# Performance work log

Measured on AMD Instinct MI355X. Metric: run time of the kernel, lower is better.

## Reference

```python
import jax, jax.numpy as jnp
import numpy as np

N = 100_000      # nodes
E = 3_200_000    # edges (before self-loops)
IN_DIM = 256
H1, H2 = 64, 32
OUT_DIM = 40
NEG_SLOPE = 0.2  # PyG GATConv default


def setup_inputs() -> dict:
    key = jax.random.key(0)
    ks = jax.random.split(key, 12)
    s = 0.05
    return {
        "x": jax.random.normal(ks[0], (N, IN_DIM), jnp.float32),
        "edge_index": jax.random.randint(ks[1], (2, E), 0, N, jnp.int32),
        "W1": jax.random.normal(ks[2], (IN_DIM, H1), jnp.float32) * s,
        "att_src1": jax.random.normal(ks[3], (H1,), jnp.float32) * s,
        "att_dst1": jax.random.normal(ks[4], (H1,), jnp.float32) * s,
        "b1": jnp.zeros((H1,), jnp.float32),
        "W2": jax.random.normal(ks[5], (H1, H2), jnp.float32) * s,
        "att_src2": jax.random.normal(ks[6], (H2,), jnp.float32) * s,
        "att_dst2": jax.random.normal(ks[7], (H2,), jnp.float32) * s,
        "b2": jnp.zeros((H2,), jnp.float32),
        "fcW": jax.random.normal(ks[8], (H2, OUT_DIM), jnp.float32) * s,
        "fcb": jnp.zeros((OUT_DIM,), jnp.float32),
    }


def gat_conv(x, src, dst, W, a_src, a_dst, b):
    """Single-head PyG GATConv (concat, heads=1). src/dst already include self-loops."""
    n = x.shape[0]
    h = x @ W                                   # [N, C] projected features (lin has no bias)
    alpha_s = (h * a_src).sum(-1)               # [N]
    alpha_d = (h * a_dst).sum(-1)               # [N]
    logit = jax.nn.leaky_relu(alpha_s[src] + alpha_d[dst], NEG_SLOPE)  # [E']
    # segment softmax over edges grouped by destination node
    m = jax.ops.segment_max(logit, dst, num_segments=n)               # [N]
    e = jnp.exp(logit - m[dst])                                        # [E']
    denom = jax.ops.segment_sum(e, dst, num_segments=n)               # [N]
    alpha = e / denom[dst]                                             # [E']
    out = jax.ops.segment_sum(h[src] * alpha[:, None], dst, num_segments=n)  # [N, C]
    return out + b


def reference(x, edge_index, W1, att_src1, att_dst1, b1, W2, att_src2, att_dst2, b2, fcW, fcb):
    n = x.shape[0]
    # add_self_loops=True (PyG GATConv default)
    loop = jnp.arange(n, dtype=edge_index.dtype)
    src = jnp.concatenate([edge_index[0], loop])
    dst = jnp.concatenate([edge_index[1], loop])
    h = jax.nn.relu(gat_conv(x, src, dst, W1, att_src1, att_dst1, b1))
    emb = jax.nn.relu(gat_conv(h, src, dst, W2, att_src2, att_dst2, b2))
    logits = emb @ fcW + fcb
    return emb, logits
```

## Files before the change

### kernel.cpp

```cpp
#include <hip/hip_runtime.h>
#include <hip/hip_bf16.h>

#define NEG_SLOPE 0.2f
#define IN_DIM 256
#define C1 64
#define C2 32
#define ODIM 40
#define SCAN_CHUNK 4096
#define BSHIFT 12
#define ECHUNK 8192
#define ECH2 16384
#define CH 10

typedef unsigned short ushort16;

__device__ __forceinline__ unsigned bf16_rne(float f) {
    unsigned a = __float_as_uint(f);
    return (a + 0x7FFFu + ((a >> 16) & 1u)) >> 16;
}
__device__ __forceinline__ void bf16x2_unpack(unsigned u, float& f0, float& f1) {
    f0 = __uint_as_float(u << 16);
    f1 = __uint_as_float(u & 0xFFFF0000u);
}


__global__ void k_bhist(const int* __restrict__ dst, int E, int* __restrict__ gh,
                        int nblk, int nb) {
    __shared__ int h[32];
    int t = threadIdx.x;
    if (t < 32) h[t] = 0;
    __syncthreads();
    int base = blockIdx.x * ECHUNK;
    int end = min(base + ECHUNK, E);
    for (int i = base + t; i < end; i += 256) atomicAdd(&h[dst[i] >> BSHIFT], 1);
    __syncthreads();
    if (t < nb) gh[t * nblk + blockIdx.x] = h[t];
}

__global__ void k_bscan(int* __restrict__ gh, int L) {
    __shared__ int lds[256];
    __shared__ int carry;
    int t = threadIdx.x;
    if (t == 0) carry = 0;
    __syncthreads();
    for (int base = 0; base < L; base += 256) {
        int v = (base + t < L) ? gh[base + t] : 0;
        lds[t] = v; __syncthreads();
        for (int off = 1; off < 256; off <<= 1) {
            int u = (t >= off) ? lds[t - off] : 0;
            __syncthreads();
            lds[t] += u;
            __syncthreads();
        }
        if (base + t < L) gh[base + t] = lds[t] - v + carry;
        __syncthreads();
        if (t == 0) carry += lds[255];
        __syncthreads();
    }
}

__global__ void k_bplace(const int* __restrict__ src, const int* __restrict__ dst, int E,
                         const int* __restrict__ gh, int nblk, int nb,
                         int2* __restrict__ pairs) {
    __shared__ int cur[32];
    int t = threadIdx.x;
    if (t < nb) cur[t] = gh[t * nblk + blockIdx.x];
    __syncthreads();
    int base = blockIdx.x * ECHUNK;
    int end = min(base + ECHUNK, E);
    for (int i = base + t; i < end; i += 256) {
        int d = dst[i];
        int pos = atomicAdd(&cur[d >> BSHIFT], 1);
        pairs[pos] = make_int2(src[i], d);
    }
}

__device__ __forceinline__ void bc_map(int blk, int* b, int* c) {
    int xcd = blk & 7, k = blk >> 3;
    *b = (k & 3) * 8 + xcd;
    *c = k >> 2;
}

__global__ __launch_bounds__(512)
void k_nhist(const int2* __restrict__ pairs, const int* __restrict__ gh, int nblk,
             int nb, int E, int* __restrict__ chist) {
    __shared__ int h[4096];
    int b, c; bc_map(blockIdx.x, &b, &c);
    if (b >= nb) return;
    for (int i = threadIdx.x; i < 4096; i += 512) h[i] = 0;
    __syncthreads();
    int estart = gh[b * nblk];
    int eend = (b + 1 < nb) ? gh[(b + 1) * nblk] : E;
    int s0 = estart + c * ECH2;
    int s1 = min(s0 + ECH2, eend);
    for (int i = s0 + threadIdx.x; i < s1; i += 512)
        atomicAdd(&h[pairs[i].y & 4095], 1);
    __syncthreads();
    int* out = chist + ((size_t)b * CH + c) * 4096;
    for (int i = threadIdx.x; i < 4096; i += 512) out[i] = h[i];
}

__global__ void k_cnt(const int* __restrict__ chist, int* __restrict__ cnt, int n) {
    int i = blockIdx.x * 256 + threadIdx.x;
    if (i >= n) return;
    int b = i >> BSHIFT, j = i & 4095;
    const int* p = chist + ((size_t)b * CH) * 4096 + j;
    int s = 1;
#pragma unroll
    for (int c = 0; c < CH; c++) s += p[c * 4096];
    cnt[i] = s;
}

__global__ void k_scan1(const int* __restrict__ cnt, int n, int* __restrict__ bsums) {
    __shared__ int lds[256];
    int t = threadIdx.x;
    int base = blockIdx.x * SCAN_CHUNK + t * 16;
    int s = 0;
#pragma unroll
    for (int i = 0; i < 16; i++) { int idx = base + i; s += (idx < n) ? cnt[idx] : 0; }
    lds[t] = s; __syncthreads();
    for (int off = 128; off > 0; off >>= 1) {
        if (t < off) lds[t] += lds[t + off];
        __syncthreads();
    }
    if (t == 0) bsums[blockIdx.x] = lds[0];
}

__global__ void k_scan2(int* bsums, int nb, int* row_ptr, int n, int total) {
    __shared__ int lds[256];
    int t = threadIdx.x;
    int v = (t < nb) ? bsums[t] : 0;
    lds[t] = v; __syncthreads();
    for (int off = 1; off < 256; off <<= 1) {
        int u = (t >= off) ? lds[t - off] : 0;
        __syncthreads();
        lds[t] += u;
        __syncthreads();
    }
    if (t < nb) bsums[t] = lds[t] - v;
    if (t == 0) row_ptr[n] = total;
}

__global__ void k_scan3(const int* __restrict__ cnt, int n, const int* __restrict__ bsums,
                        int* __restrict__ row_ptr) {
    __shared__ int lds[256];
    int t = threadIdx.x;
    int base = blockIdx.x * SCAN_CHUNK + t * 16;
    int loc[16];
    int s = 0;
#pragma unroll
    for (int i = 0; i < 16; i++) {
        int idx = base + i;
        int c = (idx < n) ? cnt[idx] : 0;
        loc[i] = s; s += c;
    }
    lds[t] = s; __syncthreads();
    for (int off = 1; off < 256; off <<= 1) {
        int u = (t >= off) ? lds[t - off] : 0;
        __syncthreads();
        lds[t] += u;
        __syncthreads();
    }
    int texcl = lds[t] - s + bsums[blockIdx.x];
#pragma unroll
    for (int i = 0; i < 16; i++) {
        int idx = base + i;
        if (idx < n) row_ptr[idx] = texcl + loc[i];
    }
}

__global__ void k_selfloop(const int* __restrict__ row_ptr, int n, int* __restrict__ adj) {
    int i = blockIdx.x * 256 + threadIdx.x;
    if (i < n) adj[row_ptr[i]] = i;
}

__global__ void k_nscan(int* __restrict__ chist, const int* __restrict__ row_ptr, int n) {
    int i = blockIdx.x * 256 + threadIdx.x;
    if (i >= n) return;
    int b = i >> BSHIFT, j = i & 4095;
    int* p = chist + ((size_t)b * CH) * 4096 + j;
    int s = row_ptr[i] + 1;
#pragma unroll
    for (int c = 0; c < CH; c++) { int t = p[c * 4096]; p[c * 4096] = s; s += t; }
}

__global__ __launch_bounds__(512)
void k_place2(const int2* __restrict__ pairs, const int* __restrict__ gh, int nblk,
              int nb, int E, const int* __restrict__ chist, int* __restrict__ adj) {
    __shared__ int cur[4096];
    int b, c; bc_map(blockIdx.x, &b, &c);
    if (b >= nb) return;
    const int* cs = chist + ((size_t)b * CH + c) * 4096;
    for (int i = threadIdx.x; i < 4096; i += 512) cur[i] = cs[i];
    __syncthreads();
    int estart = gh[b * nblk];
    int eend = (b + 1 < nb) ? gh[(b + 1) * nblk] : E;
    int s0 = estart + c * ECH2;
    int s1 = min(s0 + ECH2, eend);
    for (int i = s0 + threadIdx.x; i < s1; i += 512) {
        int2 p = pairs[i];
        int pos = atomicAdd(&cur[p.y & 4095], 1);
        adj[pos] = p.x;
    }
}


__global__ __launch_bounds__(256, 4)
void k_gemm1(const float* __restrict__ x, const float* __restrict__ W1,
             const float* __restrict__ attS, const float* __restrict__ attD,
             ushort16* __restrict__ h1b, float* __restrict__ asP,
             float* __restrict__ adP, int n) {
    int t = threadIdx.x;
    int wave = t >> 6, lane = t & 63;
    int half = blockIdx.x & 1;
    int chalf = half * 32;
    int row = (blockIdx.x >> 1) * 256 + wave * 64 + lane;
    bool active = row < n;
    int rowc = active ? row : n - 1;
    const float4* xr = (const float4*)(x + (size_t)rowc * IN_DIM);

    float acc[32];
#pragma unroll
    for (int c = 0; c < 32; c++) acc[c] = 0.f;

#define FMA_K(XC, KK) { \
        const float* wk = wb + (KK) * C1; \
        _Pragma("unroll") \
        for (int c = 0; c < 32; c++) acc[c] = fmaf((XC), wk[c], acc[c]); }

    for (int k0 = 0; k0 < 16; k0++) {
        float4 xv0 = xr[k0 * 4 + 0];
        float4 xv1 = xr[k0 * 4 + 1];
        float4 xv2 = xr[k0 * 4 + 2];
        float4 xv3 = xr[k0 * 4 + 3];
        const float* wb = W1 + (size_t)(k0 * 16) * C1 + chalf;
        FMA_K(xv0.x, 0)  FMA_K(xv0.y, 1)  FMA_K(xv0.z, 2)  FMA_K(xv0.w, 3)
        FMA_K(xv1.x, 4)  FMA_K(xv1.y, 5)  FMA_K(xv1.z, 6)  FMA_K(xv1.w, 7)
        FMA_K(xv2.x, 8)  FMA_K(xv2.y, 9)  FMA_K(xv2.z, 10) FMA_K(xv2.w, 11)
        FMA_K(xv3.x, 12) FMA_K(xv3.y, 13) FMA_K(xv3.z, 14) FMA_K(xv3.w, 15)
    }
#undef FMA_K

    if (!active) return;
    float vs = 0.f, vd = 0.f;
#pragma unroll
    for (int c = 0; c < 32; c++) {
        vs = fmaf(acc[c], attS[chalf + c], vs);
        vd = fmaf(acc[c], attD[chalf + c], vd);
    }
    asP[half * n + row] = vs;
    adP[half * n + row] = vd;

    uint4* hp = (uint4*)((ushort16*)h1b + (size_t)row * C1 + chalf);
#pragma unroll
    for (int j = 0; j < 4; j++) {
        unsigned p0 = bf16_rne(acc[j*8+0]) | (bf16_rne(acc[j*8+1]) << 16);
        unsigned p1 = bf16_rne(acc[j*8+2]) | (bf16_rne(acc[j*8+3]) << 16);
        unsigned p2 = bf16_rne(acc[j*8+4]) | (bf16_rne(acc[j*8+5]) << 16);
        unsigned p3 = bf16_rne(acc[j*8+6]) | (bf16_rne(acc[j*8+7]) << 16);
        hp[j] = make_uint4(p0, p1, p2, p3);
    }
}

__global__ void k_alphaC(const float* __restrict__ asP, const float* __restrict__ adP,
                         float* __restrict__ as1, float* __restrict__ ad1, int n) {
    int i = blockIdx.x * 256 + threadIdx.x;
    if (i < n) {
        as1[i] = asP[i] + asP[n + i];
        ad1[i] = adP[i] + adP[n + i];
    }
}


__global__ __launch_bounds__(256)
void k_agg1(const ushort16* __restrict__ h1b, const float* __restrict__ as1,
            const float* __restrict__ ad1, const int* __restrict__ row_ptr,
            const int* __restrict__ adj, const float* __restrict__ b1,
            float* __restrict__ h1out, int n) {
    int wave = (blockIdx.x * 256 + threadIdx.x) >> 6;
    int lane = threadIdx.x & 63;
    if (wave >= n) return;
    int d = wave;
    int beg = row_ptr[d], end = row_ptr[d + 1];
    float adv = ad1[d];
    int g = lane >> 3, cq = lane & 7;
    float acc[8];
#pragma unroll
    for (int k = 0; k < 8; k++) acc[k] = 0.f;
    float dsum = 0.f;

#define AGG1_ROUND(E_) { \
        int se = __shfl(s, (E_)); \
        float we = __shfl(w, (E_)); \
        uint4 u = ((const uint4*)(h1b + (size_t)se * C1))[cq]; \
        float f0, f1; \
        bf16x2_unpack(u.x, f0, f1); acc[0]=fmaf(we,f0,acc[0]); acc[1]=fmaf(we,f1,acc[1]); \
        bf16x2_unpack(u.y, f0, f1); acc[2]=fmaf(we,f0,acc[2]); acc[3]=fmaf(we,f1,acc[3]); \
        bf16x2_unpack(u.z, f0, f1); acc[4]=fmaf(we,f0,acc[4]); acc[5]=fmaf(we,f1,acc[5]); \
        bf16x2_unpack(u.w, f0, f1); acc[6]=fmaf(we,f0,acc[6]); acc[7]=fmaf(we,f1,acc[7]); }

    for (int base = beg; base < end; base += 64) {
        int cnt = min(64, end - base);
        int s = d; float w = 0.f;
        if (lane < cnt) {
            s = adj[base + lane];
            float lg = as1[s] + adv;
            lg = lg > 0.f ? lg : NEG_SLOPE * lg;
            w = expf(lg);
            dsum += w;
        }
        int j = 0;
        for (; j + 32 <= cnt; j += 32) {
            AGG1_ROUND(j + g)
            AGG1_ROUND(j + 8 + g)
            AGG1_ROUND(j + 16 + g)
            AGG1_ROUND(j + 24 + g)
        }
        for (; j < cnt; j += 8) AGG1_ROUND(j + g)
    }
#undef AGG1_ROUND

#pragma unroll
    for (int off = 32; off > 0; off >>= 1) dsum += __shfl_xor(dsum, off);
#pragma unroll
    for (int off = 8; off <= 32; off <<= 1) {
#pragma unroll
        for (int k = 0; k < 8; k++) acc[k] += __shfl_xor(acc[k], off);
    }
    if (g == 0) {
        float inv = 1.f / dsum;
        float4 bv0 = ((const float4*)b1)[cq * 2];
        float4 bv1 = ((const float4*)b1)[cq * 2 + 1];
        float4 o0, o1;
        o0.x = acc[0] * inv + bv0.x; o0.x = o0.x > 0.f ? o0.x : 0.f;
        o0.y = acc[1] * inv + bv0.y; o0.y = o0.y > 0.f ? o0.y : 0.f;
        o0.z = acc[2] * inv + bv0.z; o0.z = o0.z > 0.f ? o0.z : 0.f;
        o0.w = acc[3] * inv + bv0.w; o0.w = o0.w > 0.f ? o0.w : 0.f;
        o1.x = acc[4] * inv + bv1.x; o1.x = o1.x > 0.f ? o1.x : 0.f;
        o1.y = acc[5] * inv + bv1.y; o1.y = o1.y > 0.f ? o1.y : 0.f;
        o1.z = acc[6] * inv + bv1.z; o1.z = o1.z > 0.f ? o1.z : 0.f;
        o1.w = acc[7] * inv + bv1.w; o1.w = o1.w > 0.f ? o1.w : 0.f;
        float4* op = (float4*)(h1out + (size_t)d * C1 + cq * 8);
        op[0] = o0; op[1] = o1;
    }
}


__global__ __launch_bounds__(256)
void k_gemm2(const float* __restrict__ h1out, const float* __restrict__ W2,
             const float* __restrict__ attS, const float* __restrict__ attD,
             ushort16* __restrict__ h2b, float* __restrict__ as2,
             float* __restrict__ ad2, int n) {
    __shared__ float w2t[C2 * 68];
    __shared__ float sAttS[C2], sAttD[C2];
    int t = threadIdx.x;
    for (int i = t; i < C1 * C2; i += 256) {
        int k = i >> 5, c = i & 31;
        w2t[c * 68 + k] = W2[i];
    }
    if (t < C2) { sAttS[t] = attS[t]; sAttD[t] = attD[t]; }
    __syncthreads();
    int wave = t >> 6, lane = t & 63;
    int col = lane & 31, half = lane >> 5;
    int rowbase = blockIdx.x * 32 + wave * 8;
    const float* wrow = &w2t[col * 68];
    for (int rr = 0; rr < 8; rr += 2) {
        int row = rowbase + rr + half;
        if (row >= n) return;
        float acc = 0.f;
#pragma unroll
        for (int k = 0; k < C1; k += 4) {
            float4 wv = *(const float4*)&wrow[k];
            float4 xv = *(const float4*)&h1out[(size_t)row * C1 + k];
            acc = fmaf(xv.x, wv.x, acc);
            acc = fmaf(xv.y, wv.y, acc);
            acc = fmaf(xv.z, wv.z, acc);
            acc = fmaf(xv.w, wv.w, acc);
        }
        h2b[(size_t)row * C2 + col] = (ushort16)bf16_rne(acc);
        float vs = acc * sAttS[col], vd = acc * sAttD[col];
#pragma unroll
        for (int off = 16; off > 0; off >>= 1) {
            vs += __shfl_xor(vs, off);
            vd += __shfl_xor(vd, off);
        }
        if (col == 0) { as2[row] = vs; ad2[row] = vd; }
    }
}


__global__ __launch_bounds__(256)
void k_agg2(const ushort16* __restrict__ h2b, const float* __restrict__ as2,
            const float* __restrict__ ad2, const int* __restrict__ row_ptr,
            const int* __restrict__ adj, const float* __restrict__ b2,
            float* __restrict__ emb, int n) {
    int wave = (blockIdx.x * 256 + threadIdx.x) >> 6;
    int lane = threadIdx.x & 63;
    if (wave >= n) return;
    int d = wave;
    int beg = row_ptr[d], end = row_ptr[d + 1];
    float adv = ad2[d];
    int g = lane >> 2, cq = lane & 3;
    float acc[8];
#pragma unroll
    for (int k = 0; k < 8; k++) acc[k] = 0.f;
    float dsum = 0.f;

#define AGG2_ROUND(E_) { \
        int se = __shfl(s, (E_)); \
        float we = __shfl(w, (E_)); \
        uint4 u = ((const uint4*)(h2b + (size_t)se * C2))[cq]; \
        float f0, f1; \
        bf16x2_unpack(u.x, f0, f1); acc[0]=fmaf(we,f0,acc[0]); acc[1]=fmaf(we,f1,acc[1]); \
        bf16x2_unpack(u.y, f0, f1); acc[2]=fmaf(we,f0,acc[2]); acc[3]=fmaf(we,f1,acc[3]); \
        bf16x2_unpack(u.z, f0, f1); acc[4]=fmaf(we,f0,acc[4]); acc[5]=fmaf(we,f1,acc[5]); \
        bf16x2_unpack(u.w, f0, f1); acc[6]=fmaf(we,f0,acc[6]); acc[7]=fmaf(we,f1,acc[7]); }

    for (int base = beg; base < end; base += 64) {
        int cnt = min(64, end - base);
        int s = d; float w = 0.f;
        if (lane < cnt) {
            s = adj[base + lane];
            float lg = as2[s] + adv;
            lg = lg > 0.f ? lg : NEG_SLOPE * lg;
            w = expf(lg);
            dsum += w;
        }
        int j = 0;
        for (; j + 64 <= cnt; j += 64) {
            AGG2_ROUND(j + g)
            AGG2_ROUND(j + 16 + g)
            AGG2_ROUND(j + 32 + g)
            AGG2_ROUND(j + 48 + g)
        }
        for (; j < cnt; j += 16) AGG2_ROUND(j + g)
    }
#undef AGG2_ROUND

#pragma unroll
    for (int off = 32; off > 0; off >>= 1) dsum += __shfl_xor(dsum, off);
#pragma unroll
    for (int off = 4; off <= 32; off <<= 1) {
#pragma unroll
        for (int k = 0; k < 8; k++) acc[k] += __shfl_xor(acc[k], off);
    }
    if (g == 0) {
        float inv = 1.f / dsum;
        float4 bv0 = ((const float4*)b2)[cq * 2];
        float4 bv1 = ((const float4*)b2)[cq * 2 + 1];
        float4 o0, o1;
        o0.x = acc[0] * inv + bv0.x; o0.x = o0.x > 0.f ? o0.x : 0.f;
        o0.y = acc[1] * inv + bv0.y; o0.y = o0.y > 0.f ? o0.y : 0.f;
        o0.z = acc[2] * inv + bv0.z; o0.z = o0.z > 0.f ? o0.z : 0.f;
        o0.w = acc[3] * inv + bv0.w; o0.w = o0.w > 0.f ? o0.w : 0.f;
        o1.x = acc[4] * inv + bv1.x; o1.x = o1.x > 0.f ? o1.x : 0.f;
        o1.y = acc[5] * inv + bv1.y; o1.y = o1.y > 0.f ? o1.y : 0.f;
        o1.z = acc[6] * inv + bv1.z; o1.z = o1.z > 0.f ? o1.z : 0.f;
        o1.w = acc[7] * inv + bv1.w; o1.w = o1.w > 0.f ? o1.w : 0.f;
        float4* op = (float4*)(emb + (size_t)d * C2 + cq * 8);
        op[0] = o0; op[1] = o1;
    }
}


__global__ __launch_bounds__(256)
void k_logits(const float* __restrict__ emb, const float* __restrict__ fcW,
              const float* __restrict__ fcb, float* __restrict__ out, int n) {
    __shared__ float w[C2 * ODIM];
    __shared__ float b[ODIM];
    int t = threadIdx.x;
    for (int i = t; i < C2 * ODIM; i += 256) w[i] = fcW[i];
    if (t < ODIM) b[t] = fcb[t];
    __syncthreads();
    int lane = t & 63;
    int row = blockIdx.x * 4 + (t >> 6);
    if (row >= n) return;
    float acc = (lane < ODIM) ? b[lane] : 0.f;
    const float4* er = (const float4*)&emb[(size_t)row * C2];
#pragma unroll
    for (int c4 = 0; c4 < 8; c4++) {
        float4 e = er[c4];
        int c = c4 * 4;
        if (lane < ODIM) {
            acc = fmaf(e.x, w[(c + 0) * ODIM + lane], acc);
            acc = fmaf(e.y, w[(c + 1) * ODIM + lane], acc);
            acc = fmaf(e.z, w[(c + 2) * ODIM + lane], acc);
            acc = fmaf(e.w, w[(c + 3) * ODIM + lane], acc);
        }
    }
    if (lane < ODIM) out[(size_t)row * ODIM + lane] = acc;
}


extern "C" void kernel_launch(void* const* d_in, const int* in_sizes, int n_in,
                              void* d_out, int out_size, void* d_ws, size_t ws_size,
                              hipStream_t stream) {
    const float* x    = (const float*)d_in[0];
    const int*   ei   = (const int*)d_in[1];
    const float* W1   = (const float*)d_in[2];
    const float* aS1  = (const float*)d_in[3];
    const float* aD1  = (const float*)d_in[4];
    const float* b1   = (const float*)d_in[5];
    const float* W2   = (const float*)d_in[6];
    const float* aS2  = (const float*)d_in[7];
    const float* aD2  = (const float*)d_in[8];
    const float* b2   = (const float*)d_in[9];
    const float* fcW  = (const float*)d_in[10];
    const float* fcb  = (const float*)d_in[11];

    const int N = in_sizes[0] / IN_DIM;
    const int E = in_sizes[1] / 2;
    const int* src = ei;
    const int* dst = ei + E;

    ushort16* h1b = (ushort16*)d_ws;
    float* h1out  = (float*)((char*)d_ws + (size_t)N * C1 * 2);
    float* as1    = h1out + (size_t)N * C1;
    float* ad1    = as1 + N;
    float* as2    = ad1 + N;
    float* ad2    = as2 + N;
    float* asP    = ad2 + N;
    float* adP    = asP + 2 * (size_t)N;
    int*   cnt    = (int*)(adP + 2 * (size_t)N);
    int*   row_ptr = cnt + N;
    int*   bsums   = row_ptr + (N + 1);
    int*   adj     = bsums + 256;
    int*   gh      = adj + (E + N);

    int2* pairs = (int2*)h1out;
    int*  chist = (int*)h1b;
    ushort16* h2b = (ushort16*)h1b;

    float* emb    = (float*)d_out;
    float* logits = emb + (size_t)N * C2;

    int nbN   = (N + 255) / 256;
    int nbS   = (N + SCAN_CHUNK - 1) / SCAN_CHUNK;
    int nblkE = (E + ECHUNK - 1) / ECHUNK;
    int nb    = (N + (1 << BSHIFT) - 1) >> BSHIFT;
    int nBC   = 8 * 4 * CH;

    k_bhist<<<nblkE, 256, 0, stream>>>(dst, E, gh, nblkE, nb);
    k_bscan<<<1, 256, 0, stream>>>(gh, nb * nblkE);
    k_bplace<<<nblkE, 256, 0, stream>>>(src, dst, E, gh, nblkE, nb, pairs);
    k_nhist<<<nBC, 512, 0, stream>>>(pairs, gh, nblkE, nb, E, chist);
    k_cnt<<<nbN, 256, 0, stream>>>(chist, cnt, N);
    k_scan1<<<nbS, 256, 0, stream>>>(cnt, N, bsums);
    k_scan2<<<1, 256, 0, stream>>>(bsums, nbS, row_ptr, N, E + N);
    k_scan3<<<nbS, 256, 0, stream>>>(cnt, N, bsums, row_ptr);
    k_selfloop<<<nbN, 256, 0, stream>>>(row_ptr, N, adj);
    k_nscan<<<nbN, 256, 0, stream>>>(chist, row_ptr, N);
    k_place2<<<nBC, 512, 0, stream>>>(pairs, gh, nblkE, nb, E, chist, adj);

    int nbG1 = 2 * ((N + 255) / 256);
    k_gemm1<<<nbG1, 256, 0, stream>>>(x, W1, aS1, aD1, h1b, asP, adP, N);
    k_alphaC<<<nbN, 256, 0, stream>>>(asP, adP, as1, ad1, N);
    int nbA = (N + 3) / 4;
    k_agg1<<<nbA, 256, 0, stream>>>(h1b, as1, ad1, row_ptr, adj, b1, h1out, N);
    int nbG2 = (N + 31) / 32;
    k_gemm2<<<nbG2, 256, 0, stream>>>(h1out, W2, aS2, aD2, h2b, as2, ad2, N);
    k_agg2<<<nbA, 256, 0, stream>>>(h2b, as2, ad2, row_ptr, adj, b2, emb, N);
    k_logits<<<nbA, 256, 0, stream>>>(emb, fcW, fcb, logits, N);
}
```

Before: 409.7 us.

## Stage x tiles in LDS so both column halves share one global read

```diff
diff --git a/kernel.cpp b/kernel.cpp
--- a/kernel.cpp
+++ b/kernel.cpp
@@ -210,36 +210,51 @@
              const float* __restrict__ attS, const float* __restrict__ attD,
              ushort16* __restrict__ h1b, float* __restrict__ asP,
              float* __restrict__ adP, int n) {
+    __shared__ float xs[128 * 33];
     int t = threadIdx.x;
     int wave = t >> 6, lane = t & 63;
-    int half = blockIdx.x & 1;
+    int rhalf = wave >> 1;
+    int half = wave & 1;
     int chalf = half * 32;
-    int row = (blockIdx.x >> 1) * 256 + wave * 64 + lane;
+    int row0 = blockIdx.x * 128;
+    int row = row0 + rhalf * 64 + lane;
     bool active = row < n;
-    int rowc = active ? row : n - 1;
-    const float4* xr = (const float4*)(x + (size_t)rowc * IN_DIM);
 
     float acc[32];
 #pragma unroll
     for (int c = 0; c < 32; c++) acc[c] = 0.f;
 
-#define FMA_K(XC, KK) { \
-        const float* wk = wb + (KK) * C1; \
-        _Pragma("unroll") \
-        for (int c = 0; c < 32; c++) acc[c] = fmaf((XC), wk[c], acc[c]); }
-
-    for (int k0 = 0; k0 < 16; k0++) {
-        float4 xv0 = xr[k0 * 4 + 0];
-        float4 xv1 = xr[k0 * 4 + 1];
-        float4 xv2 = xr[k0 * 4 + 2];
-        float4 xv3 = xr[k0 * 4 + 3];
-        const float* wb = W1 + (size_t)(k0 * 16) * C1 + chalf;
-        FMA_K(xv0.x, 0)  FMA_K(xv0.y, 1)  FMA_K(xv0.z, 2)  FMA_K(xv0.w, 3)
-        FMA_K(xv1.x, 4)  FMA_K(xv1.y, 5)  FMA_K(xv1.z, 6)  FMA_K(xv1.w, 7)
-        FMA_K(xv2.x, 8)  FMA_K(xv2.y, 9)  FMA_K(xv2.z, 10) FMA_K(xv2.w, 11)
-        FMA_K(xv3.x, 12) FMA_K(xv3.y, 13) FMA_K(xv3.z, 14) FMA_K(xv3.w, 15)
-    }
-#undef FMA_K
+    for (int k0 = 0; k0 < IN_DIM; k0 += 32) {
+        if (k0) __syncthreads();
+#pragma unroll
+        for (int i = 0; i < 4; i++) {
+            int fid = i * 256 + t;
+            int r = fid >> 3;
+            int kk = (fid & 7) * 4;
+            int gr = row0 + r; if (gr >= n) gr = n - 1;
+            float4 v = *(const float4*)&x[(size_t)gr * IN_DIM + k0 + kk];
+            float* xp = &xs[r * 33 + kk];
+            xp[0] = v.x; xp[1] = v.y; xp[2] = v.z; xp[3] = v.w;
+        }
+        __syncthreads();
+        const float* xrow = &xs[(rhalf * 64 + lane) * 33];
+#pragma unroll
+        for (int kk = 0; kk < 32; kk += 4) {
+            float x0 = xrow[kk + 0];
+            float x1 = xrow[kk + 1];
+            float x2 = xrow[kk + 2];
+            float x3 = xrow[kk + 3];
+            const float* wb = W1 + (size_t)(k0 + kk) * C1 + chalf;
+#pragma unroll
+            for (int c = 0; c < 32; c++) acc[c] = fmaf(x0, wb[c], acc[c]);
+#pragma unroll
+            for (int c = 0; c < 32; c++) acc[c] = fmaf(x1, wb[C1 + c], acc[c]);
+#pragma unroll
+            for (int c = 0; c < 32; c++) acc[c] = fmaf(x2, wb[2 * C1 + c], acc[c]);
+#pragma unroll
+            for (int c = 0; c < 32; c++) acc[c] = fmaf(x3, wb[3 * C1 + c], acc[c]);
+        }
+    }
 
     if (!active) return;
     float vs = 0.f, vd = 0.f;
@@ -248,8 +263,8 @@
         vs = fmaf(acc[c], attS[chalf + c], vs);
         vd = fmaf(acc[c], attD[chalf + c], vd);
     }
-    asP[half * n + row] = vs;
-    adP[half * n + row] = vd;
+    asP[(size_t)half * n + row] = vs;
+    adP[(size_t)half * n + row] = vd;
 
     uint4* hp = (uint4*)((ushort16*)h1b + (size_t)row * C1 + chalf);
 #pragma unroll
@@ -266,8 +281,8 @@
                          float* __restrict__ as1, float* __restrict__ ad1, int n) {
     int i = blockIdx.x * 256 + threadIdx.x;
     if (i < n) {
-        as1[i] = asP[i] + asP[n + i];
-        ad1[i] = adP[i] + adP[n + i];
+        as1[i] = asP[i] + asP[(size_t)n + i];
+        ad1[i] = adP[i] + adP[(size_t)n + i];
     }
 }
 
@@ -552,7 +567,7 @@
     k_nscan<<<nbN, 256, 0, stream>>>(chist, row_ptr, N);
     k_place2<<<nBC, 512, 0, stream>>>(pairs, gh, nblkE, nb, E, chist, adj);
 
-    int nbG1 = 2 * ((N + 255) / 256);
+    int nbG1 = (N + 127) / 128;
     k_gemm1<<<nbG1, 256, 0, stream>>>(x, W1, aS1, aD1, h1b, asP, adP, N);
     k_alphaC<<<nbN, 256, 0, stream>>>(asP, adP, as1, ad1, N);
     int nbA = (N + 3) / 4;
```

Measured after the change: 1.171 ms. 186% more time.
